# Kernel optimization log

Hardware: AMD Instinct MI355X
Metric: run time of the kernel (lower is better)

## Reference

```python
import jax, jax.numpy as jnp
import numpy as np
import math

D_MODEL, N_HEADS, BATCH, SEQ = 1024, 16, 2, 2048
D_HEAD = D_MODEL // N_HEADS


def setup_inputs() -> dict:
    key = jax.random.key(0)
    ks = jax.random.split(key, 5)
    w = lambda k: jax.random.normal(k, (D_MODEL, D_MODEL), jnp.float32) * 0.02
    return {
        "X": jax.random.normal(ks[0], (BATCH, SEQ, D_MODEL), jnp.float32),
        "W_q": w(ks[1]),
        "W_k": w(ks[2]),
        "W_v": w(ks[3]),
        "W_o": w(ks[4]),
        "g_q": jnp.ones((D_MODEL,), jnp.float32),
        "b_q": jnp.zeros((D_MODEL,), jnp.float32),
        "g_k": jnp.ones((D_MODEL,), jnp.float32),
        "b_k": jnp.zeros((D_MODEL,), jnp.float32),
        "cache_k": jnp.zeros((BATCH, N_HEADS, SEQ, D_HEAD), jnp.float32),
        "cache_v": jnp.zeros((BATCH, N_HEADS, SEQ, D_HEAD), jnp.float32),
        "start_pos": 0,
    }


def _layernorm(x, g, b, eps=1e-5):
    mu = jnp.mean(x, axis=-1, keepdims=True)
    xc = x - mu
    var = jnp.mean(xc * xc, axis=-1, keepdims=True)
    return xc * jax.lax.rsqrt(var + eps) * g + b


def reference(X, W_q, W_k, W_v, W_o, g_q, b_q, g_k, b_k, cache_k, cache_v, start_pos):
    batch, N, d_model = X.shape
    H = cache_k.shape[1]
    dh = d_model // H

    # QK-normed projections (torch Linear: x @ W^T)
    XQ = _layernorm(X @ W_q.T, g_q, b_q)
    XK = _layernorm(X @ W_k.T, g_k, b_k)
    XV = X @ W_v.T
    split = lambda t: t.reshape(batch, N, H, dh).transpose(0, 2, 1, 3)  # [b,h,n,d]
    XQ, XK, XV = split(XQ), split(XK), split(XV)

    # KV-cache scatter update, then slice to valid prefix (start_pos is static)
    cache_k = jax.lax.dynamic_update_slice(cache_k, XK, (0, 0, start_pos, 0))
    cache_v = jax.lax.dynamic_update_slice(cache_v, XV, (0, 0, start_pos, 0))
    M = start_pos + N
    K = cache_k[:, :, :M]
    V = cache_v[:, :, :M]

    logits = jnp.einsum('bhnd,bhmd->bhnm', XQ, K) / math.sqrt(dh)  # [b,h,N,M]

    # causal mask on the freshly written block [start_pos:M]
    tril = jnp.tril(jnp.ones((N, N), bool))
    full_mask = jnp.concatenate([jnp.ones((N, start_pos), bool), tril], axis=1)  # [N,M]
    logits = jnp.where(full_mask[None, None], logits, -jnp.inf)

    # selective forget-mask bias built from relu'd head-0 logits
    S = jax.nn.relu(logits[:, 0])               # relu(-inf) -> 0, matches torch
    S = S.at[..., 0].set(0.0)                   # zero first column
    S = S * (1.0 - jnp.eye(N, dtype=S.dtype))   # zero diagonal (valid since start_pos==0)
    S = jnp.roll(S, 1, axis=-2)                 # shift rows down by one
    S = S.at[..., 0, :].set(0.0)
    F_mask = jnp.cumsum(S, axis=-2)             # [b,N,M]

    logits = logits - F_mask[:, None]
    attn = jax.nn.softmax(logits, axis=-1)
    O = jnp.einsum('bhnm,bhmd->bhnd', attn, V)
    O = O.transpose(0, 2, 1, 3).reshape(batch, N, d_model)
    return O @ W_o.T
```

## Files before the change

kernel.cpp:

```cpp
#include <hip/hip_runtime.h>
#include <cstdint>
#include <cstddef>


typedef unsigned short u16;
typedef __attribute__((ext_vector_type(8))) __bf16 bf16x8;
typedef __attribute__((ext_vector_type(4))) float f32x4;
typedef __attribute__((ext_vector_type(2))) unsigned int uint2v;

#define D_MODEL 1024
#define N_HEADS 16
#define BATCH   2
#define SEQ     2048
#define D_HEAD  64
#define ROWS    (BATCH*SEQ)
#define NSEG    64
#define SEGLEN  32
#define LOG2E   1.44269504f

static __device__ __forceinline__ u16 f2bf(float f){
  union { float f; uint32_t u; } v; v.f = f;
  uint32_t r = v.u + 0x7fffu + ((v.u >> 16) & 1u);
  return (u16)(r >> 16);
}
static __device__ __forceinline__ float bf2f(u16 h){
  union { uint32_t u; float f; } v; v.u = ((uint32_t)h) << 16;
  return v.f;
}
static __device__ __forceinline__ uint32_t pack2(float a, float b){
  uint32_t ua = __float_as_uint(a) + 0x8000u;
  uint32_t ub = __float_as_uint(b) + 0x8000u;
  return (ua >> 16) | (ub & 0xffff0000u);
}
#define GLDS(gp, lp) __builtin_amdgcn_global_load_lds( \
    (const __attribute__((address_space(1))) void*)(gp), \
    (__attribute__((address_space(3))) void*)(lp), 16, 0, 0)

__global__ void k_cast_all(const float* __restrict__ X,
                           u16* __restrict__ Xhi, u16* __restrict__ Xlo,
                           const float* __restrict__ Wq,
                           u16* __restrict__ Wqh, u16* __restrict__ Wql,
                           const float* __restrict__ Wk,
                           u16* __restrict__ Wkh, u16* __restrict__ Wkl,
                           const float* __restrict__ Wv, u16* __restrict__ Wvb,
                           const float* __restrict__ Wo, u16* __restrict__ Wob){
  int i = blockIdx.x*256 + threadIdx.x;
  if (i < 1572864){
    const float* src; u16 *dh, *dl; int base;
    if (i < 1048576){ src = X;  dh = Xhi; dl = Xlo; base = i; }
    else if (i < 1310720){ src = Wq; dh = Wqh; dl = Wql; base = i - 1048576; }
    else { src = Wk; dh = Wkh; dl = Wkl; base = i - 1310720; }
    float4 v = reinterpret_cast<const float4*>(src)[base];
    float vs[4] = {v.x, v.y, v.z, v.w};
    union { u16 s[4]; uint2 u; } uh, ul;
#pragma unroll
    for (int r=0;r<4;++r){
      uh.s[r] = f2bf(vs[r]);
      ul.s[r] = f2bf(vs[r] - bf2f(uh.s[r]));
    }
    reinterpret_cast<uint2*>(dh)[base] = uh.u;
    reinterpret_cast<uint2*>(dl)[base] = ul.u;
  } else {
    const float* src; u16* dst; int base;
    if (i < 1835008){ src = Wv; dst = Wvb; base = i - 1572864; }
    else { src = Wo; dst = Wob; base = i - 1835008; }
    float4 v = reinterpret_cast<const float4*>(src)[base];
    float vs[4] = {v.x, v.y, v.z, v.w};
    union { u16 s[4]; uint2 u; } uh;
#pragma unroll
    for (int r=0;r<4;++r) uh.s[r] = f2bf(vs[r]);
    reinterpret_cast<uint2*>(dst)[base] = uh.u;
  }
}

__global__ __launch_bounds__(256) void k_mega(
    const u16* __restrict__ Xhi, const u16* __restrict__ Xlo,
    const u16* __restrict__ Wh,  const u16* __restrict__ Wl,
    const u16* __restrict__ Wvb,
    float* __restrict__ C, float* __restrict__ Dlt, u16* __restrict__ Vt)
{
  __shared__ __align__(16) u16 smem[16384];
  const int bid = blockIdx.x;
  const int tid = threadIdx.x, wv = tid>>6, ln = tid&63;
  const int lane15 = ln&15, quad = ln>>4;
  const int wm = wv&1, wn = wv>>1;
  const int g = ln&7, sr = ln>>3;
  const int fs = lane15 & 7;
  f32x4 z = {0.f,0.f,0.f,0.f};
  u16* As = smem;
  u16* Bs = smem + 8192;

  if (bid < 128){
    const int cx = bid & 1;
    const int cy = (bid >> 1) & 31;
    const int cz = bid >> 6;
    const size_t rowBase = (size_t)cy*128;
    const size_t wbase = cx ? (size_t)1024*1024 : 0;
    const u16* Ap = cz ? Xlo : Xhi;
    const u16* Bp = (cz ? Wh : Wl) + wbase;
    f32x4 acc[4][2];
#pragma unroll
    for (int i=0;i<4;++i){ acc[i][0] = z; acc[i][1] = z; }
    for (int kt = 0; kt < 16; ++kt) {
      __syncthreads();
#pragma unroll
      for (int c = 0; c < 4; ++c) {
        int chunk = wv*4 + c, r = chunk*8 + sr;
        GLDS(Ap + (rowBase + r)*1024 + kt*64 + (g^sr)*8, As + chunk*512);
      }
#pragma unroll
      for (int c = 0; c < 2; ++c) {
        int chunk = wv*2 + c, r = chunk*8 + sr;
        GLDS(Bp + (size_t)r*1024 + kt*64 + (g^sr)*8, Bs + chunk*512);
      }
      __syncthreads();
#pragma unroll
      for (int k2=0;k2<2;++k2){
        bf16x8 af[4], bfb[2];
#pragma unroll
        for (int t=0;t<4;++t)
          af[t]  = *reinterpret_cast<const bf16x8*>(As + (wm*64 + t*16 + lane15)*64 + (((k2*4+quad)^fs)*8));
#pragma unroll
        for (int t=0;t<2;++t)
          bfb[t] = *reinterpret_cast<const bf16x8*>(Bs + (wn*32 + t*16 + lane15)*64 + (((k2*4+quad)^fs)*8));
#pragma unroll
        for (int i=0;i<4;++i)
#pragma unroll
          for (int j=0;j<2;++j)
            acc[i][j] = __builtin_amdgcn_mfma_f32_16x16x32_bf16(af[i], bfb[j], acc[i][j], 0,0,0);
      }
    }
#pragma unroll
    for (int i=0;i<4;++i){
      size_t row = rowBase + wm*64 + i*16 + quad*4;
#pragma unroll
      for (int j=0;j<2;++j){
        size_t col = (size_t)cx*64 + wn*32 + j*16 + lane15;
#pragma unroll
        for (int r=0;r<4;++r)
          atomicAdd(&Dlt[(row+r)*128 + col], acc[i][j][r]);
      }
    }
  } else if (bid < 640){
    const int idx = bid - 128;
    const size_t rowBase = (size_t)(idx>>4)*128, colBase = (size_t)(idx&15)*128;
    f32x4 acc[4][4];
#pragma unroll
    for (int i=0;i<4;++i)
#pragma unroll
      for (int j=0;j<4;++j) acc[i][j] = z;
    for (int kt = 0; kt < 16; ++kt) {
      __syncthreads();
#pragma unroll
      for (int c = 0; c < 4; ++c) {
        int chunk = wv*4 + c, r = chunk*8 + sr;
        GLDS(Xhi + (rowBase + r)*1024 + kt*64 + (g^sr)*8, As + chunk*512);
        GLDS(Wh  + (colBase + r)*1024 + kt*64 + (g^sr)*8, Bs + chunk*512);
      }
      __syncthreads();
#pragma unroll
      for (int k2=0;k2<2;++k2){
        bf16x8 af[4], bfb[4];
#pragma unroll
        for (int t=0;t<4;++t){
          af[t]  = *reinterpret_cast<const bf16x8*>(As + (wm*64 + t*16 + lane15)*64 + (((k2*4+quad)^fs)*8));
          bfb[t] = *reinterpret_cast<const bf16x8*>(Bs + (wn*64 + t*16 + lane15)*64 + (((k2*4+quad)^fs)*8));
        }
#pragma unroll
        for (int i=0;i<4;++i)
#pragma unroll
          for (int j=0;j<4;++j)
            acc[i][j] = __builtin_amdgcn_mfma_f32_16x16x32_bf16(af[i], bfb[j], acc[i][j], 0,0,0);
      }
    }
#pragma unroll
    for (int i=0;i<4;++i){
      size_t row = rowBase + wm*64 + i*16 + quad*4;
#pragma unroll
      for (int j=0;j<4;++j){
        size_t col = colBase + wn*64 + j*16 + lane15;
#pragma unroll
        for (int r=0;r<4;++r)
          C[(row+r)*2048 + col] = acc[i][j][r];
      }
    }
  } else {
    const int idx = bid - 640;
    const int bx = idx & 15, by = idx >> 4;
    const size_t rowBase = (size_t)by*128, colBase = (size_t)bx*64;
    f32x4 acc[4][2];
#pragma unroll
    for (int i=0;i<4;++i){ acc[i][0] = z; acc[i][1] = z; }
    for (int kt = 0; kt < 16; ++kt) {
      __syncthreads();
#pragma unroll
      for (int c = 0; c < 4; ++c) {
        int chunk = wv*4 + c, r = chunk*8 + sr;
        GLDS(Xhi + (rowBase + r)*1024 + kt*64 + (g^sr)*8, As + chunk*512);
      }
#pragma unroll
      for (int c = 0; c < 2; ++c) {
        int chunk = wv*2 + c, r = chunk*8 + sr;
        GLDS(Wvb + (colBase + r)*1024 + kt*64 + (g^sr)*8, Bs + chunk*512);
      }
      __syncthreads();
#pragma unroll
      for (int k2=0;k2<2;++k2){
        bf16x8 af[4], bfb[2];
#pragma unroll
        for (int t=0;t<4;++t)
          af[t]  = *reinterpret_cast<const bf16x8*>(As + (wm*64 + t*16 + lane15)*64 + (((k2*4+quad)^fs)*8));
#pragma unroll
        for (int t=0;t<2;++t)
          bfb[t] = *reinterpret_cast<const bf16x8*>(Bs + (wn*32 + t*16 + lane15)*64 + (((k2*4+quad)^fs)*8));
#pragma unroll
        for (int i=0;i<4;++i)
#pragma unroll
          for (int j=0;j<2;++j)
            acc[i][j] = __builtin_amdgcn_mfma_f32_16x16x32_bf16(af[i], bfb[j], acc[i][j], 0,0,0);
      }
    }
    __syncthreads();
#pragma unroll
    for (int i=0;i<4;++i){
      int nl = wm*64 + i*16 + quad*4;
#pragma unroll
      for (int j=0;j<2;++j){
        int dl = wn*32 + j*16 + lane15;
#pragma unroll
        for (int r=0;r<4;++r)
          smem[dl*136 + nl + r] = f2bf(acc[i][j][r]);
      }
    }
    __syncthreads();
    const int b = by >> 4;
    const int n0 = (by & 15) * 128;
    const int bh = b*N_HEADS + bx;
    const int d = tid >> 2, seg = tid & 3;
    u16* dst = Vt + ((size_t)(bh*64 + d))*SEQ + n0 + seg*32;
    const u16* srcl = smem + d*136 + seg*32;
#pragma unroll
    for (int k=0;k<4;++k)
      *reinterpret_cast<uint4*>(dst + k*8) = *reinterpret_cast<const uint4*>(srcl + k*8);
  }
}

__global__ __launch_bounds__(256) void k_ln_pack2(
    const float* __restrict__ C, const float* __restrict__ Dlt,
    const float* __restrict__ gq, const float* __restrict__ bq,
    const float* __restrict__ gk, const float* __restrict__ bk,
    u16* __restrict__ Qh, u16* __restrict__ Kh,
    u16* __restrict__ Q0l, u16* __restrict__ K0l)
{
  const int row = blockIdx.x;
  const int tid = threadIdx.x;
  const float* cr = C + (size_t)row*2048;
  float4 vq = reinterpret_cast<const float4*>(cr)[tid];
  float4 vk = reinterpret_cast<const float4*>(cr)[256 + tid];
  const int h = tid >> 4;
  if (h == 0){
    float4 dq = reinterpret_cast<const float4*>(Dlt + (size_t)row*128)[tid&15];
    vq.x+=dq.x; vq.y+=dq.y; vq.z+=dq.z; vq.w+=dq.w;
    float4 dk = reinterpret_cast<const float4*>(Dlt + (size_t)row*128 + 64)[tid&15];
    vk.x+=dk.x; vk.y+=dk.y; vk.z+=dk.z; vk.w+=dk.w;
  }
  float sq  = vq.x+vq.y+vq.z+vq.w;
  float s2q = vq.x*vq.x+vq.y*vq.y+vq.z*vq.z+vq.w*vq.w;
  float sk  = vk.x+vk.y+vk.z+vk.w;
  float s2k = vk.x*vk.x+vk.y*vk.y+vk.z*vk.z+vk.w*vk.w;
#pragma unroll
  for (int o=32;o;o>>=1){
    sq += __shfl_xor(sq,o);  s2q += __shfl_xor(s2q,o);
    sk += __shfl_xor(sk,o);  s2k += __shfl_xor(s2k,o);
  }
  __shared__ float red[4][4];
  if ((tid&63)==0){
    red[tid>>6][0]=sq; red[tid>>6][1]=s2q; red[tid>>6][2]=sk; red[tid>>6][3]=s2k;
  }
  __syncthreads();
  sq  = red[0][0]+red[1][0]+red[2][0]+red[3][0];
  s2q = red[0][1]+red[1][1]+red[2][1]+red[3][1];
  sk  = red[0][2]+red[1][2]+red[2][2]+red[3][2];
  s2k = red[0][3]+red[1][3]+red[2][3]+red[3][3];
  const float muq = sq*(1.f/D_MODEL);
  const float rsq = rsqrtf(s2q*(1.f/D_MODEL) - muq*muq + 1e-5f);
  const float muk = sk*(1.f/D_MODEL);
  const float rsk = rsqrtf(s2k*(1.f/D_MODEL) - muk*muk + 1e-5f);
  const int b = row >> 11, n = row & (SEQ-1);
  const int d0 = (tid & 15)*4;
  float4 gqv = reinterpret_cast<const float4*>(gq)[tid];
  float4 bqv = reinterpret_cast<const float4*>(bq)[tid];
  float4 gkv = reinterpret_cast<const float4*>(gk)[tid];
  float4 bkv = reinterpret_cast<const float4*>(bk)[tid];
  float xq[4] = {vq.x,vq.y,vq.z,vq.w}, xk[4] = {vk.x,vk.y,vk.z,vk.w};
  float gQ[4] = {gqv.x,gqv.y,gqv.z,gqv.w}, bQ[4] = {bqv.x,bqv.y,bqv.z,bqv.w};
  float gK[4] = {gkv.x,gkv.y,gkv.z,gkv.w}, bK[4] = {bkv.x,bkv.y,bkv.z,bkv.w};
  union { u16 s[4]; uint2 u; } qh, ql, kh, kl;
#pragma unroll
  for (int r=0;r<4;++r){
    float yq = (xq[r]-muq)*rsq*gQ[r] + bQ[r];
    qh.s[r] = f2bf(yq);
    ql.s[r] = f2bf(yq - bf2f(qh.s[r]));
    float yk = (xk[r]-muk)*rsk*gK[r] + bK[r];
    kh.s[r] = f2bf(yk);
    kl.s[r] = f2bf(yk - bf2f(kh.s[r]));
  }
  size_t dst = (((size_t)(b*N_HEADS + h))*SEQ + n)*D_HEAD + d0;
  *reinterpret_cast<uint2*>(Qh + dst) = qh.u;
  *reinterpret_cast<uint2*>(Kh + dst) = kh.u;
  if (h == 0){
    size_t dl = ((size_t)b*SEQ + n)*D_HEAD + d0;
    *reinterpret_cast<uint2*>(Q0l + dl) = ql.u;
    *reinterpret_cast<uint2*>(K0l + dl) = kl.u;
  }
}

__global__ __launch_bounds__(256) void k_s0(
    const u16* Qh, const u16* Q0l, const u16* Kh, const u16* K0l,
    float* __restrict__ S0, float* __restrict__ seg)
{
  const int b = blockIdx.z;
  const int bm = blockIdx.y;
  const int bn = blockIdx.x;
  const int tid = threadIdx.x;
  if (bn > bm){
    for (int t = tid; t < 512; t += 256)
      seg[((size_t)b*NSEG + bm*4 + (t>>7))*SEQ + bn*128 + (t&127)] = 0.f;
    return;
  }
  float* Sb = S0 + (size_t)b*SEQ*SEQ;
  __shared__ __align__(16) u16 smem[4*8192];
  const int wv = tid>>6, ln = tid&63;
  const int lane15 = ln&15, quad = ln>>4;
  const int wm = wv&1, wn = wv>>1;
  const int g = ln&7, sr = ln>>3;
  const int fs = lane15 & 7;
  const size_t rowBase = (size_t)bm*128, colBase = (size_t)bn*128;
  const u16* srcs[4] = {
    Qh  + ((size_t)b*N_HEADS*SEQ + rowBase)*D_HEAD,
    Q0l + ((size_t)b*SEQ + rowBase)*D_HEAD,
    Kh  + ((size_t)b*N_HEADS*SEQ + colBase)*D_HEAD,
    K0l + ((size_t)b*SEQ + colBase)*D_HEAD };
#pragma unroll
  for (int t=0;t<4;++t){
#pragma unroll
    for (int c=0;c<4;++c){
      int chunk = wv*4 + c, r = chunk*8 + sr;
      GLDS(srcs[t] + (size_t)r*64 + (g^sr)*8, smem + t*8192 + chunk*512);
    }
  }
  __syncthreads();
  f32x4 acc[4][4];
  f32x4 z = {0.f,0.f,0.f,0.f};
#pragma unroll
  for (int i=0;i<4;++i)
#pragma unroll
    for (int j=0;j<4;++j) acc[i][j] = z;
  const int Aidx[3] = {0, 0, 1};
  const int Bidx[3] = {2, 3, 2};
#pragma unroll
  for (int p = 0; p < 3; ++p){
    const u16* At = smem + Aidx[p]*8192;
    const u16* Bt = smem + Bidx[p]*8192;
#pragma unroll
    for (int k2=0;k2<2;++k2){
      bf16x8 af[4], bfb[4];
#pragma unroll
      for (int t=0;t<4;++t){
        af[t]  = *reinterpret_cast<const bf16x8*>(At + (wm*64 + t*16 + lane15)*64 + (((k2*4+quad)^fs)*8));
        bfb[t] = *reinterpret_cast<const bf16x8*>(Bt + (wn*64 + t*16 + lane15)*64 + (((k2*4+quad)^fs)*8));
      }
#pragma unroll
      for (int i=0;i<4;++i)
#pragma unroll
        for (int j=0;j<4;++j)
          acc[i][j] = __builtin_amdgcn_mfma_f32_16x16x32_bf16(af[i], bfb[j], acc[i][j], 0,0,0);
    }
  }
  float csum[2][4] = {{0.f,0.f,0.f,0.f},{0.f,0.f,0.f,0.f}};
#pragma unroll
  for (int i=0;i<4;++i){
#pragma unroll
    for (int j=0;j<4;++j){
#pragma unroll
      for (int r=0;r<4;++r){
        int jg = (int)rowBase + wm*64 + i*16 + quad*4 + r;
        int mg = (int)colBase + wn*64 + j*16 + lane15;
        float l = acc[i][j][r]*0.125f;
        float s = (mg >= 1 && mg < jg) ? fmaxf(l, 0.f) : 0.f;
        Sb[(size_t)jg*SEQ + mg] = s;
        csum[i>>1][j] += s;
      }
    }
  }
  __syncthreads();
  float* cs = (float*)smem;
#pragma unroll
  for (int h2=0;h2<2;++h2){
#pragma unroll
    for (int j=0;j<4;++j){
      float v = csum[h2][j];
      v += __shfl_xor(v, 16);
      v += __shfl_xor(v, 32);
      if (ln < 16) cs[(wm*2 + h2)*128 + wn*64 + j*16 + ln] = v;
    }
  }
  __syncthreads();
  for (int t = tid; t < 512; t += 256)
    seg[((size_t)b*NSEG + bm*4 + (t>>7))*SEQ + bn*128 + (t&127)] = cs[t];
}

__global__ void k_seg_apply(float* __restrict__ SF, const float* __restrict__ seg){
  int m = blockIdx.x*256 + threadIdx.x;
  int s = blockIdx.y, b = blockIdx.z;
  const float* sb = seg + (size_t)b*NSEG*SEQ;
  float run = 0.f;
  for (int t=0; t<s; ++t) run += sb[(size_t)t*SEQ + m];
  float* Sb = SF + (size_t)b*SEQ*SEQ;
  const int j0 = s*SEGLEN;
#pragma unroll 8
  for (int i=0;i<SEGLEN;++i){
    size_t idx = (size_t)(j0 + i)*SEQ + m;
    float t = Sb[idx];
    Sb[idx] = -run*LOG2E;
    run += (j0 + i > m) ? t : 0.f;
  }
}

__constant__ unsigned char WMAP[48] = {
  62,63,60,79,
  61,58,59,56,78,
  57,54,55,52,77,
  53,50,51,48,76,
  49,46,47,44,75,
  45,42,43,40,74,
  41,38,39,36,73,
  37,34,35,32,72,
  33,71,
  70,69,68,67,66,65,64};

__global__ __launch_bounds__(256, 4) void k_attn(
    const u16* __restrict__ Qh, const u16* __restrict__ Kh,
    const u16* __restrict__ Vt, const float* __restrict__ F,
    u16* __restrict__ Ob, float* __restrict__ Opart, float* __restrict__ Ps)
{
  __shared__ __align__(16) u16 Ks[2][64*64];
  __shared__ __align__(16) u16 Vs[2][64*64];
  const int w = blockIdx.x;
  const int bh = w & 31, b = bh >> 4, h = bh & 15;
  const int item = (int)WMAP[w >> 5];
  int nt, mt0, mt1, segi;
  if (item >= 64){ nt = item - 64; segi = 0; mt0 = 0; mt1 = nt; }
  else {
    nt = item >> 1; segi = item & 1;
    const int half = (nt + 2) >> 1;
    mt0 = segi ? half : 0;
    mt1 = segi ? nt : (half - 1);
  }
  const bool partial = (item < 64);
  const int tid = threadIdx.x, wv = tid>>6, ln = tid&63;
  const int lane15 = ln&15, quad = ln>>4;
  const u16* Qbh = Qh + ((size_t)(b*N_HEADS + h))*SEQ*D_HEAD;
  const u16* Kbh = Kh + ((size_t)(b*N_HEADS + h))*SEQ*D_HEAD;
  const u16* Vbh = Vt + ((size_t)(b*N_HEADS + h))*D_HEAD*SEQ;
  const int n_loc = wv*16 + lane15;
  const int n_g = nt*64 + n_loc;
  const float* Frow = F + (size_t)b*SEQ*SEQ + (size_t)n_g*SEQ;
  const int swz = (ln&7) ^ ((ln>>3)&7);
  const int fswz = lane15 & 7;
  const int srow = ln>>3;

  bf16x8 qf[2];
#pragma unroll
  for (int kt=0; kt<2; ++kt)
    qf[kt] = *reinterpret_cast<const bf16x8*>(Qbh + (size_t)n_g*D_HEAD + kt*32 + quad*8);

  f32x4 z = {0.f,0.f,0.f,0.f};
  f32x4 psum = z;
  f32x4 acc_o[4];
#pragma unroll
  for (int no=0;no<4;++no) acc_o[no] = z;

  auto stage = [&](int mt, int buf){
#pragma unroll
    for (int c=0;c<2;++c){
      int chunk = wv*2 + c;
      int r = chunk*8 + srow;
      GLDS(Kbh + (size_t)(mt*64 + r)*D_HEAD + swz*8, &Ks[buf][chunk*512]);
      GLDS(Vbh + (size_t)r*SEQ + mt*64 + swz*8,      &Vs[buf][chunk*512]);
    }
  };
  stage(mt0, mt0 & 1);
  f32x4 fvn[4];
#pragma unroll
  for (int ms=0; ms<4; ++ms)
    fvn[ms] = *reinterpret_cast<const f32x4*>(Frow + mt0*64 + ms*16 + quad*4);
  const float c1 = 0.125f*LOG2E;

  for (int mt = mt0; mt <= mt1; ++mt) {
    const int cur = mt & 1;
    __syncthreads();
    if (mt < mt1) stage(mt+1, 1-cur);
    f32x4 fv[4];
#pragma unroll
    for (int ms=0; ms<4; ++ms) fv[ms] = fvn[ms];
    if (mt < mt1){
      const float* Fr1 = Frow + (mt+1)*64;
#pragma unroll
      for (int ms=0; ms<4; ++ms)
        fvn[ms] = *reinterpret_cast<const f32x4*>(Fr1 + ms*16 + quad*4);
    }
    f32x4 accs[4];
#pragma unroll
    for (int ms=0;ms<4;++ms) accs[ms] = z;
    __builtin_amdgcn_s_setprio(1);
#pragma unroll
    for (int kt=0; kt<2; ++kt){
#pragma unroll
      for (int ms=0; ms<4; ++ms){
        bf16x8 a = *reinterpret_cast<const bf16x8*>(
            &Ks[cur][(ms*16 + lane15)*64 + (((kt*4 + quad) ^ fswz) * 8)]);
        accs[ms] = __builtin_amdgcn_mfma_f32_16x16x32_bf16(a, qf[kt], accs[ms], 0,0,0);
      }
    }
    __builtin_amdgcn_s_setprio(0);
    const bool diag = (mt == nt);
    uint32_t pw[4][2];
#pragma unroll
    for (int ms=0; ms<4; ++ms){
      f32x4 t = accs[ms];
      float p[4];
#pragma unroll
      for (int r=0;r<4;++r){
        float l2 = fmaf(t[r], c1, fv[ms][r]);
        if (diag){
          int ml = ms*16 + quad*4 + r;
          l2 = (ml > n_loc) ? -1e30f : l2;
        }
        p[r] = __builtin_amdgcn_exp2f(l2);
      }
      psum[0]+=p[0]; psum[1]+=p[1]; psum[2]+=p[2]; psum[3]+=p[3];
      pw[ms][0] = pack2(p[0], p[1]);
      pw[ms][1] = pack2(p[2], p[3]);
    }
    __builtin_amdgcn_s_setprio(1);
#pragma unroll
    for (int kt=0; kt<2; ++kt){
      union { uint32_t u[4]; bf16x8 v; } pa;
#pragma unroll
      for (int pr=0; pr<2; ++pr){
        uint2v s32 = __builtin_amdgcn_permlane32_swap(
            pw[2*kt][pr], pw[2*kt+1][pr], false, false);
        uint2v s16 = __builtin_amdgcn_permlane16_swap(s32.x, s32.y, false, false);
        pa.u[pr]   = s16.x;
        pa.u[2+pr] = s16.y;
      }
#pragma unroll
      for (int no=0; no<4; ++no){
        int d = no*16 + lane15;
        bf16x8 vb = *reinterpret_cast<const bf16x8*>(
            &Vs[cur][d*64 + (((kt*4 + quad) ^ (d&7)) * 8)]);
        acc_o[no] = __builtin_amdgcn_mfma_f32_16x16x32_bf16(pa.v, vb, acc_o[no], 0,0,0);
      }
    }
    __builtin_amdgcn_s_setprio(0);
  }
  float s = (psum[0]+psum[1]) + (psum[2]+psum[3]);
  s += __shfl_xor(s, 16);
  s += __shfl_xor(s, 32);
  if (partial){
    const size_t pb = (size_t)(bh*16 + (nt - 16))*2 + segi;
    float* Op = Opart + pb*4096;
    if (quad == 0) Ps[pb*64 + wv*16 + lane15] = s;
#pragma unroll
    for (int no=0; no<4; ++no)
#pragma unroll
      for (int r=0;r<4;++r)
        Op[(wv*16 + quad*4 + r)*64 + no*16 + lane15] = acc_o[no][r];
  } else {
    f32x4 inv;
#pragma unroll
    for (int r=0;r<4;++r)
      inv[r] = __builtin_amdgcn_rcpf(__shfl(s, quad*4 + r));
#pragma unroll
    for (int no=0; no<4; ++no){
#pragma unroll
      for (int r=0;r<4;++r){
        float o = acc_o[no][r] * inv[r];
        int row = nt*64 + wv*16 + quad*4 + r;
        Ob[((size_t)(b*SEQ + row))*D_MODEL + h*64 + no*16 + lane15] = f2bf(o);
      }
    }
  }
}

__global__ __launch_bounds__(256) void k_comb(
    const float* __restrict__ Opart, const float* __restrict__ Ps,
    u16* __restrict__ Ob)
{
  const int t = blockIdx.x;
  const int bh = t >> 4, b = bh >> 4, h = bh & 15;
  const int nt = (t & 15) + 16;
  const int tid = threadIdx.x;
  const int row = tid >> 2, c0 = (tid & 3) * 16;
  const float* P0 = Opart + (size_t)t*2*4096 + row*64 + c0;
  const float* P1 = P0 + 4096;
  const float s = Ps[(size_t)t*128 + row] + Ps[(size_t)t*128 + 64 + row];
  const float inv = __builtin_amdgcn_rcpf(s);
  union { u16 us[16]; uint4 u[2]; } o;
#pragma unroll
  for (int g2=0; g2<4; ++g2){
    float4 a = reinterpret_cast<const float4*>(P0)[g2];
    float4 c = reinterpret_cast<const float4*>(P1)[g2];
    o.us[g2*4+0] = f2bf((a.x + c.x) * inv);
    o.us[g2*4+1] = f2bf((a.y + c.y) * inv);
    o.us[g2*4+2] = f2bf((a.z + c.z) * inv);
    o.us[g2*4+3] = f2bf((a.w + c.w) * inv);
  }
  u16* dst = Ob + ((size_t)(b*SEQ + nt*64 + row))*D_MODEL + h*64 + c0;
  reinterpret_cast<uint4*>(dst)[0] = o.u[0];
  reinterpret_cast<uint4*>(dst)[1] = o.u[1];
}

__global__ __launch_bounds__(256) void k_gemm_nt64(
    const u16* __restrict__ A0, const u16* __restrict__ B0,
    float* __restrict__ C, int N, int K)
{
  __shared__ __align__(16) u16 As[8192];
  __shared__ __align__(16) u16 Bs[4096];
  const int tid = threadIdx.x, wv = tid>>6, ln = tid&63;
  const int lane15 = ln&15, quad = ln>>4;
  const int wm = wv&1, wn = wv>>1;
  const int g = ln&7, sr = ln>>3;
  const int fs = lane15 & 7;
  const size_t rowBase = (size_t)blockIdx.y*128, colBase = (size_t)blockIdx.x*64;
  f32x4 acc[4][2];
  f32x4 z = {0.f,0.f,0.f,0.f};
#pragma unroll
  for (int i=0;i<4;++i){ acc[i][0] = z; acc[i][1] = z; }
  const int ktiles = K >> 6;
  for (int kt = 0; kt < ktiles; ++kt) {
    __syncthreads();
#pragma unroll
    for (int c = 0; c < 4; ++c) {
      int chunk = wv*4 + c, r = chunk*8 + sr;
      GLDS(A0 + (rowBase + r)*K + kt*64 + (g^sr)*8, As + chunk*512);
    }
#pragma unroll
    for (int c = 0; c < 2; ++c) {
      int chunk = wv*2 + c, r = chunk*8 + sr;
      GLDS(B0 + (colBase + r)*K + kt*64 + (g^sr)*8, Bs + chunk*512);
    }
    __syncthreads();
#pragma unroll
    for (int k2=0;k2<2;++k2){
      bf16x8 af[4], bfb[2];
#pragma unroll
      for (int t=0;t<4;++t)
        af[t]  = *reinterpret_cast<const bf16x8*>(As + (wm*64 + t*16 + lane15)*64 + (((k2*4+quad)^fs)*8));
#pragma unroll
      for (int t=0;t<2;++t)
        bfb[t] = *reinterpret_cast<const bf16x8*>(Bs + (wn*32 + t*16 + lane15)*64 + (((k2*4+quad)^fs)*8));
#pragma unroll
      for (int i=0;i<4;++i)
#pragma unroll
        for (int j=0;j<2;++j)
          acc[i][j] = __builtin_amdgcn_mfma_f32_16x16x32_bf16(af[i], bfb[j], acc[i][j], 0,0,0);
    }
  }
#pragma unroll
  for (int i=0;i<4;++i){
    size_t row = rowBase + wm*64 + i*16 + quad*4;
#pragma unroll
    for (int j=0;j<2;++j){
      size_t col = colBase + wn*32 + j*16 + lane15;
#pragma unroll
      for (int r=0;r<4;++r)
        C[(row+r)*N + col] = acc[i][j][r];
    }
  }
}

extern "C" void kernel_launch(void* const* d_in, const int* in_sizes, int n_in,
                              void* d_out, int out_size, void* d_ws, size_t ws_size,
                              hipStream_t stream)
{
  (void)in_sizes; (void)n_in; (void)out_size; (void)ws_size;
  const float* X  = (const float*)d_in[0];
  const float* Wq = (const float*)d_in[1];
  const float* Wk = (const float*)d_in[2];
  const float* Wv = (const float*)d_in[3];
  const float* Wo = (const float*)d_in[4];
  const float* gq = (const float*)d_in[5];
  const float* bq = (const float*)d_in[6];
  const float* gk = (const float*)d_in[7];
  const float* bk = (const float*)d_in[8];
  float* out = (float*)d_out;

  char* ws = (char*)d_ws;
  size_t off = 0;
  auto alloc = [&](size_t bytes)->char*{
    char* p = ws + off; off += (bytes + 255) & ~(size_t)255; return p;
  };
  u16* Xhi  = (u16*)alloc((size_t)ROWS*D_MODEL*2);
  u16* Xlo  = (u16*)alloc((size_t)ROWS*D_MODEL*2);
  u16* Wqkh = (u16*)alloc((size_t)2*D_MODEL*D_MODEL*2);
  u16* Wqkl = (u16*)alloc((size_t)2*D_MODEL*D_MODEL*2);
  u16* Wvb  = (u16*)alloc((size_t)D_MODEL*D_MODEL*2);
  u16* Wob  = (u16*)alloc((size_t)D_MODEL*D_MODEL*2);
  u16* Qhp  = (u16*)alloc((size_t)BATCH*N_HEADS*SEQ*D_HEAD*2);
  u16* Khp  = (u16*)alloc((size_t)BATCH*N_HEADS*SEQ*D_HEAD*2);
  u16* Q0l  = (u16*)alloc((size_t)BATCH*SEQ*D_HEAD*2);
  u16* K0l  = (u16*)alloc((size_t)BATCH*SEQ*D_HEAD*2);
  u16* Vtp  = (u16*)alloc((size_t)BATCH*N_HEADS*D_HEAD*SEQ*2);
  u16* Obf  = (u16*)alloc((size_t)ROWS*D_MODEL*2);
  float* Dlt = (float*)alloc((size_t)ROWS*128*4);
  float* Seg = (float*)alloc((size_t)BATCH*NSEG*SEQ*4);
  float* Opart = (float*)alloc((size_t)512*2*4096*4);
  float* Ps    = (float*)alloc((size_t)512*2*64*4);
  float* SF  = (float*)alloc((size_t)BATCH*SEQ*SEQ*4);
  float* C32 = SF;

  hipMemsetAsync(Dlt, 0, (size_t)ROWS*128*4, stream);

  k_cast_all<<<8192, 256, 0, stream>>>(
      X, Xhi, Xlo,
      Wq, Wqkh, Wqkl,
      Wk, Wqkh + (size_t)D_MODEL*D_MODEL, Wqkl + (size_t)D_MODEL*D_MODEL,
      Wv, Wvb, Wo, Wob);
  k_mega<<<1152, 256, 0, stream>>>(Xhi, Xlo, Wqkh, Wqkl, Wvb, C32, Dlt, Vtp);
  k_ln_pack2<<<ROWS, 256, 0, stream>>>(C32, Dlt, gq, bq, gk, bk, Qhp, Khp, Q0l, K0l);
  k_s0<<<dim3(16, 16, BATCH), 256, 0, stream>>>(Qhp, Q0l, Khp, K0l, SF, Seg);
  k_seg_apply<<<dim3(8, NSEG, BATCH), 256, 0, stream>>>(SF, Seg);
  k_attn<<<1536, 256, 0, stream>>>(Qhp, Khp, Vtp, SF, Obf, Opart, Ps);
  k_comb<<<512, 256, 0, stream>>>(Opart, Ps, Obf);
  k_gemm_nt64<<<dim3(16, 32), 256, 0, stream>>>(Obf, Wob, out, D_MODEL, D_MODEL);
}
```

Before: 288.6 us.

## Replace atomic delta accumulation with split buffers, use hardware bf16 pack, raise attn occupancy

The low-precision correction GEMM now writes each of its two K-split partials to its own buffer instead of atomically adding into one zeroed buffer, and the layernorm kernel sums both partials. This removes the memset and the atomics. In the attention kernel, software bf16 packing is replaced by the v_cvt_pk_bf16_f32 instruction, and the QK loop is restructured so the first MFMA takes zero directly. Masking is split into a separate pass, and the launch-bounds occupancy hint goes from 4 to 5, which may increase register pressure or cause spills. The pack conversion also changes rounding from round-half-up to the hardware's rounding mode.

```diff
diff --git a/kernel.cpp b/kernel.cpp
--- a/kernel.cpp
+++ b/kernel.cpp
@@ -27,10 +27,10 @@
   union { uint32_t u; float f; } v; v.u = ((uint32_t)h) << 16;
   return v.f;
 }
-static __device__ __forceinline__ uint32_t pack2(float a, float b){
-  uint32_t ua = __float_as_uint(a) + 0x8000u;
-  uint32_t ub = __float_as_uint(b) + 0x8000u;
-  return (ua >> 16) | (ub & 0xffff0000u);
+static __device__ __forceinline__ uint32_t cvtpk(float lo, float hi){
+  uint32_t r;
+  asm("v_cvt_pk_bf16_f32 %0, %1, %2" : "=v"(r) : "v"(lo), "v"(hi));
+  return r;
 }
 #define GLDS(gp, lp) __builtin_amdgcn_global_load_lds( \
     (const __attribute__((address_space(1))) void*)(gp), \
@@ -130,6 +130,7 @@
             acc[i][j] = __builtin_amdgcn_mfma_f32_16x16x32_bf16(af[i], bfb[j], acc[i][j], 0,0,0);
       }
     }
+    float* Dp = Dlt + (size_t)cz*ROWS*128;
 #pragma unroll
     for (int i=0;i<4;++i){
       size_t row = rowBase + wm*64 + i*16 + quad*4;
@@ -138,7 +139,7 @@
         size_t col = (size_t)cx*64 + wn*32 + j*16 + lane15;
 #pragma unroll
         for (int r=0;r<4;++r)
-          atomicAdd(&Dlt[(row+r)*128 + col], acc[i][j][r]);
+          Dp[(row+r)*128 + col] = acc[i][j][r];
       }
     }
   } else if (bid < 640){
@@ -259,10 +260,14 @@
   float4 vk = reinterpret_cast<const float4*>(cr)[256 + tid];
   const int h = tid >> 4;
   if (h == 0){
-    float4 dq = reinterpret_cast<const float4*>(Dlt + (size_t)row*128)[tid&15];
-    vq.x+=dq.x; vq.y+=dq.y; vq.z+=dq.z; vq.w+=dq.w;
-    float4 dk = reinterpret_cast<const float4*>(Dlt + (size_t)row*128 + 64)[tid&15];
-    vk.x+=dk.x; vk.y+=dk.y; vk.z+=dk.z; vk.w+=dk.w;
+    const float* D0 = Dlt + (size_t)row*128;
+    const float* D1 = Dlt + (size_t)ROWS*128 + (size_t)row*128;
+    float4 a0 = reinterpret_cast<const float4*>(D0)[tid&15];
+    float4 a1 = reinterpret_cast<const float4*>(D1)[tid&15];
+    vq.x+=a0.x+a1.x; vq.y+=a0.y+a1.y; vq.z+=a0.z+a1.z; vq.w+=a0.w+a1.w;
+    float4 b0 = reinterpret_cast<const float4*>(D0 + 64)[tid&15];
+    float4 b1 = reinterpret_cast<const float4*>(D1 + 64)[tid&15];
+    vk.x+=b0.x+b1.x; vk.y+=b0.y+b1.y; vk.z+=b0.z+b1.z; vk.w+=b0.w+b1.w;
   }
   float sq  = vq.x+vq.y+vq.z+vq.w;
   float s2q = vq.x*vq.x+vq.y*vq.y+vq.z*vq.z+vq.w*vq.w;
@@ -439,7 +444,7 @@
   33,71,
   70,69,68,67,66,65,64};
 
-__global__ __launch_bounds__(256, 4) void k_attn(
+__global__ __launch_bounds__(256, 5) void k_attn(
     const u16* __restrict__ Qh, const u16* __restrict__ Kh,
     const u16* __restrict__ Vt, const float* __restrict__ F,
     u16* __restrict__ Ob, float* __restrict__ Opart, float* __restrict__ Ps)
@@ -511,37 +516,45 @@
         fvn[ms] = *reinterpret_cast<const f32x4*>(Fr1 + ms*16 + quad*4);
     }
     f32x4 accs[4];
-#pragma unroll
-    for (int ms=0;ms<4;++ms) accs[ms] = z;
     __builtin_amdgcn_s_setprio(1);
 #pragma unroll
-    for (int kt=0; kt<2; ++kt){
-#pragma unroll
-      for (int ms=0; ms<4; ++ms){
-        bf16x8 a = *reinterpret_cast<const bf16x8*>(
-            &Ks[cur][(ms*16 + lane15)*64 + (((kt*4 + quad) ^ fswz) * 8)]);
-        accs[ms] = __builtin_amdgcn_mfma_f32_16x16x32_bf16(a, qf[kt], accs[ms], 0,0,0);
-      }
+    for (int ms=0; ms<4; ++ms){
+      bf16x8 a = *reinterpret_cast<const bf16x8*>(
+          &Ks[cur][(ms*16 + lane15)*64 + ((quad ^ fswz) * 8)]);
+      accs[ms] = __builtin_amdgcn_mfma_f32_16x16x32_bf16(a, qf[0], z, 0,0,0);
+    }
+#pragma unroll
+    for (int ms=0; ms<4; ++ms){
+      bf16x8 a = *reinterpret_cast<const bf16x8*>(
+          &Ks[cur][(ms*16 + lane15)*64 + (((4 + quad) ^ fswz) * 8)]);
+      accs[ms] = __builtin_amdgcn_mfma_f32_16x16x32_bf16(a, qf[1], accs[ms], 0,0,0);
     }
     __builtin_amdgcn_s_setprio(0);
-    const bool diag = (mt == nt);
+    float l2[4][4];
+#pragma unroll
+    for (int ms=0; ms<4; ++ms)
+#pragma unroll
+      for (int r=0; r<4; ++r)
+        l2[ms][r] = fmaf(accs[ms][r], c1, fv[ms][r]);
+    if (mt == nt){
+#pragma unroll
+      for (int ms=0; ms<4; ++ms)
+#pragma unroll
+        for (int r=0; r<4; ++r){
+          int ml = ms*16 + quad*4 + r;
+          if (ml > n_loc) l2[ms][r] = -1e30f;
+        }
+    }
     uint32_t pw[4][2];
 #pragma unroll
     for (int ms=0; ms<4; ++ms){
-      f32x4 t = accs[ms];
-      float p[4];
-#pragma unroll
-      for (int r=0;r<4;++r){
-        float l2 = fmaf(t[r], c1, fv[ms][r]);
-        if (diag){
-          int ml = ms*16 + quad*4 + r;
-          l2 = (ml > n_loc) ? -1e30f : l2;
-        }
-        p[r] = __builtin_amdgcn_exp2f(l2);
-      }
-      psum[0]+=p[0]; psum[1]+=p[1]; psum[2]+=p[2]; psum[3]+=p[3];
-      pw[ms][0] = pack2(p[0], p[1]);
-      pw[ms][1] = pack2(p[2], p[3]);
+      float p0 = __builtin_amdgcn_exp2f(l2[ms][0]);
+      float p1 = __builtin_amdgcn_exp2f(l2[ms][1]);
+      float p2 = __builtin_amdgcn_exp2f(l2[ms][2]);
+      float p3 = __builtin_amdgcn_exp2f(l2[ms][3]);
+      psum[0]+=p0; psum[1]+=p1; psum[2]+=p2; psum[3]+=p3;
+      pw[ms][0] = cvtpk(p0, p1);
+      pw[ms][1] = cvtpk(p2, p3);
     }
     __builtin_amdgcn_s_setprio(1);
 #pragma unroll
@@ -714,14 +727,12 @@
   u16* K0l  = (u16*)alloc((size_t)BATCH*SEQ*D_HEAD*2);
   u16* Vtp  = (u16*)alloc((size_t)BATCH*N_HEADS*D_HEAD*SEQ*2);
   u16* Obf  = (u16*)alloc((size_t)ROWS*D_MODEL*2);
-  float* Dlt = (float*)alloc((size_t)ROWS*128*4);
+  float* Dlt = (float*)alloc((size_t)2*ROWS*128*4);
   float* Seg = (float*)alloc((size_t)BATCH*NSEG*SEQ*4);
   float* Opart = (float*)alloc((size_t)512*2*4096*4);
   float* Ps    = (float*)alloc((size_t)512*2*64*4);
   float* SF  = (float*)alloc((size_t)BATCH*SEQ*SEQ*4);
   float* C32 = SF;
-
-  hipMemsetAsync(Dlt, 0, (size_t)ROWS*128*4, stream);
 
   k_cast_all<<<8192, 256, 0, stream>>>(
       X, Xhi, Xlo,
```

Result: slower. 306.8 us (+6.3%).
